# Performance work log

Measured on AMD Instinct MI355X. Metric: run time of the kernel, lower is better.

The kernel has to match this reference:

```python
import jax, jax.numpy as jnp
import numpy as np

B, T, NH, NB = 16, 400, 100, 65
SR, BLOCK = 16000, 160
REV_LEN = SR  # Reverb(sampling_rate, sampling_rate)


def _fft_convolve(signal, kernel):
    # torch: pad signal right by n, kernel left by its length, multiply spectra, keep 2nd half
    n = signal.shape[-1]
    s = jnp.pad(signal, [(0, 0)] * (signal.ndim - 1) + [(0, n)])
    k = jnp.pad(kernel, [(0, 0)] * (kernel.ndim - 1) + [(kernel.shape[-1], 0)])
    out = jnp.fft.irfft(jnp.fft.rfft(s) * jnp.fft.rfft(k), s.shape[-1])
    return out[..., out.shape[-1] // 2:]


def _amp_to_impulse_response(amp, target_size):
    # amp: [..., n_bands] real magnitudes treated as zero-phase rfft coefficients
    ir = jnp.fft.irfft(jax.lax.complex(amp, jnp.zeros_like(amp)))  # [..., 2*(NB-1)]
    fs = ir.shape[-1]
    ir = jnp.roll(ir, fs // 2, axis=-1)
    win = 0.5 - 0.5 * jnp.cos(2.0 * np.pi * jnp.arange(fs, dtype=ir.dtype) / fs)  # periodic hann
    ir = ir * win
    ir = jnp.pad(ir, [(0, 0)] * (ir.ndim - 1) + [(0, target_size - fs)])
    return jnp.roll(ir, -fs // 2, axis=-1)


def setup_inputs() -> dict:
    key = jax.random.key(0)
    ks = jax.random.split(key, 6)
    pitch = 40.0 + 400.0 * jax.random.uniform(ks[0], (B, T, 1), dtype=jnp.float32)
    total_amp = jax.random.uniform(ks[1], (B, T), dtype=jnp.float32)
    harmo_amps = jax.random.uniform(ks[2], (B, NH, T), dtype=jnp.float32) + 1e-3
    noise_filter = 0.1 * jax.random.uniform(ks[3], (B, T, NB), dtype=jnp.float32)
    noise = 2.0 * jax.random.uniform(ks[4], (B, T, BLOCK), dtype=jnp.float32) - 1.0
    reverb_noise = 2.0 * jax.random.uniform(ks[5], (REV_LEN, 1), dtype=jnp.float32) - 1.0
    decay = jnp.asarray(5.0, jnp.float32)
    wet = jnp.asarray(0.0, jnp.float32)
    return dict(pitch=pitch, total_amp=total_amp, harmo_amps=harmo_amps,
                noise_filter=noise_filter, noise=noise, reverb_noise=reverb_noise,
                decay=decay, wet=wet, sampling_rate=SR, block_size=BLOCK)


def reference(pitch, total_amp, harmo_amps, noise_filter, noise, reverb_noise,
              decay, wet, sampling_rate, block_size):
    dt = pitch.dtype
    n_harm = harmo_amps.shape[1]
    harm_idx = jnp.arange(1, n_harm + 1, dtype=dt)
    # remove_above_nyquist: mask harmonics whose freq >= sr/2 (tiny epsilon kept, as in DDSP)
    freqs = pitch[:, :, 0][:, None, :] * harm_idx[None, :, None]          # [B,NH,T]
    aa = (freqs < (sampling_rate / 2)).astype(dt) + 1e-4
    amps = harmo_amps * aa
    amps = jnp.transpose(amps, (0, 2, 1))                                  # [B,T,NH]
    amps = amps / jnp.sum(amps, axis=-1, keepdims=True)
    amps = amps * total_amp[..., None]
    # nearest-neighbor upsample by block_size (F.interpolate default mode)
    amps_up = jnp.repeat(amps, block_size, axis=1)                         # [B,N,NH]
    pitch_up = jnp.repeat(pitch, block_size, axis=1)                       # [B,N,1]
    # harmonic additive synthesis
    omega = jnp.cumsum(2.0 * np.pi * pitch_up / sampling_rate, axis=1)     # [B,N,1]
    harmonic = jnp.sum(jnp.sin(omega * harm_idx) * amps_up, axis=-1, keepdims=True)
    # filtered noise branch
    impulse = _amp_to_impulse_response(noise_filter, block_size)           # [B,T,BLOCK]
    noise_f = _fft_convolve(noise, impulse)                                # [B,T,BLOCK]
    noise_f = noise_f.reshape(noise_f.shape[0], -1, 1)                     # [B,N,1]
    signal = harmonic + noise_f
    # reverb (forward with reverb=True)
    rev_len = reverb_noise.shape[0]
    t = (jnp.arange(rev_len, dtype=dt) / sampling_rate)[None, :, None]     # [1,L,1]
    imp = reverb_noise[None] * jnp.exp(-jax.nn.softplus(-decay) * t * 500.0) * jax.nn.sigmoid(wet)
    imp = imp.at[:, 0].set(1.0)
    imp = jnp.pad(imp, ((0, 0), (0, signal.shape[1] - rev_len), (0, 0)))   # [1,N,1]
    out = _fft_convolve(signal[..., 0], imp[..., 0])[..., None]            # [B,N,1]
    return out
```

## Files before the change

### kernel.cpp

```cpp
#include <hip/hip_runtime.h>

#define B_ 16
#define T_ 400
#define NH_ 100
#define NB_ 65
#define BLK_ 160
#define SR_ 16000
#define N_ 64000
#define REV_ 16000
#define KPAD_ 16128
#define KTOT_ 80128
#define M_ 16
#define NWG_ 250
#define ISTRIDE_ 16768

typedef __attribute__((ext_vector_type(8))) _Float16 f16x8;
typedef __attribute__((ext_vector_type(2))) _Float16 f16x2;
typedef __attribute__((ext_vector_type(4))) float f32x4;
typedef __attribute__((ext_vector_type(4))) unsigned uint4v;
typedef uint4v __attribute__((aligned(4))) uint4v_a4;

static __device__ __forceinline__ float dot2f(f16x2 a, f16x2 b, float c) {
#if __has_builtin(__builtin_amdgcn_fdot2)
  return __builtin_amdgcn_fdot2(a, b, c, false);
#else
  return fmaf((float)a[0], (float)b[0], fmaf((float)a[1], (float)b[1], c));
#endif
}

__global__ __launch_bounds__(512) void k_pre(const float* __restrict__ pitch,
                                             const float* __restrict__ rn,
                                             const float* __restrict__ dec,
                                             const float* __restrict__ wet,
                                             double* __restrict__ Pv,
                                             double* __restrict__ Xv,
                                             _Float16* __restrict__ IMPREV,
                                             _Float16* __restrict__ PH) {
  const int blk = blockIdx.x, tid = threadIdx.x;
  if (blk < 66) {
    const int gid = blk * 512 + tid;
    if (gid < 2 * ISTRIDE_) {
      const int c = gid / ISTRIDE_, u = gid - c * ISTRIDE_;
      const int i = 16383 - u - c;
      float v = 0.f;
      if (i == 0) {
        v = 1.0f;
      } else if (i > 0 && i < REV_) {
        const float a = log1pf(expf(-dec[0]));
        const float sg = 1.f / (1.f + expf(-wet[0]));
        v = rn[i] * expf(-a * ((float)i / (float)SR_) * 500.0f) * sg;
      }
      IMPREV[gid] = (_Float16)v;
    }
    return;
  }
  if (blk < 129) {
    const int gid = (blk - 66) * 512 + tid;
    ((f32x4*)PH)[gid] = (f32x4){0.f, 0.f, 0.f, 0.f};
    return;
  }
  __shared__ double s[512];
  const int b = blk - 129, t = tid;
  double x = 0.0;
  if (t < T_) x = (double)pitch[b * T_ + t] * (1.0 / (double)SR_);
  s[t] = x;
  __syncthreads();
  for (int off = 1; off < 512; off <<= 1) {
    double v = (t >= off) ? s[t - off] : 0.0;
    __syncthreads();
    s[t] += v;
    __syncthreads();
  }
  if (t < T_) {
    Xv[b * T_ + t] = x;
    Pv[b * T_ + t] = (s[t] - x) * 160.0;
  }
}

__global__ __launch_bounds__(320) void k_synth(
    const float* __restrict__ pitch, const float* __restrict__ tamp,
    const float* __restrict__ harmo, const float* __restrict__ nfilt,
    const float* __restrict__ noise, const double* __restrict__ Pv,
    const double* __restrict__ Xv, _Float16* __restrict__ PH) {
  const int tid = threadIdx.x;
  const int g = (tid >= 160) ? 1 : 0;
  const int ltid = tid - (g << 7) - (g << 5);
  const int bt = (blockIdx.x << 1) + g;
  const int b = bt / T_, t = bt - b * T_;
  __shared__ __align__(16) float amp[2][112];
  __shared__ __align__(16) float a_s[2][68];
  __shared__ __align__(16) float ir_s[2][68];
  __shared__ __align__(16) _Float16 C0[2][320];
  __shared__ __align__(16) _Float16 C1[2][320];
  __shared__ __align__(16) _Float16 imp_sw[2][128];
  __shared__ float red_s[2];

  const float pv = pitch[bt];
  int nv = (int)(8000.0f / pv);
  if (nv > NH_) nv = NH_;
  while (nv < NH_ && (float)(nv + 1) * pv < 8000.0f) ++nv;
  while (nv > 0 && (float)nv * pv >= 8000.0f) --nv;

  if (ltid < NB_) a_s[g][ltid] = nfilt[bt * NB_ + ltid];
  {
    const _Float16 nh = (_Float16)noise[bt * BLK_ + ltid];
    C0[g][160 + ltid] = nh;
    C1[g][159 + ltid] = nh;
    C0[g][ltid] = (_Float16)0.f;
    if (ltid < 159) C1[g][ltid] = (_Float16)0.f;
  }
  if (ltid < NH_) {
    const float ha = harmo[(b * NH_ + ltid) * T_ + t];
    const float aa = (pv * (float)(ltid + 1) < 8000.0f ? 1.0f : 0.0f) + 1e-4f;
    amp[g][ltid] = ha * aa;
  } else if (ltid < 112) {
    amp[g][ltid] = 0.f;
  }
  __syncthreads();

  float irv = 0.f;
  if (ltid < 65) {
    const float phi = (float)ltid * (1.0f / 128.0f);
    const float c1 = __builtin_amdgcn_cosf(phi);
    const float c2 = fmaf(2.f * c1, c1, -1.f);
    const float c3 = fmaf(2.f * c2, c1, -c1);
    const float c4 = fmaf(2.f * c2, c2, -1.f);
    const float tc = 2.f * c4;
    float x0 = 1.f, p0 = c4;
    float x1 = c1, p1 = c3;
    float x2 = c2, p2 = c2;
    float x3 = c3, p3 = c1;
    float a0 = 0.f, a1 = 0.f, a2 = 0.f, a3 = 0.f;
#pragma unroll
    for (int m = 0; m < 8; ++m) {
      const f32x4 aA = *(const f32x4*)&a_s[g][m << 3];
      const f32x4 aB = *(const f32x4*)&a_s[g][(m << 3) + 4];
      a0 = fmaf(aA[0], x0, a0); const float y0 = fmaf(tc, x0, -p0);
      a1 = fmaf(aA[1], x1, a1); const float y1 = fmaf(tc, x1, -p1);
      a2 = fmaf(aA[2], x2, a2); const float y2 = fmaf(tc, x2, -p2);
      a3 = fmaf(aA[3], x3, a3); const float y3 = fmaf(tc, x3, -p3);
      a0 = fmaf(aB[0], y0, a0); const float z0 = fmaf(tc, y0, -x0); p0 = y0; x0 = z0;
      a1 = fmaf(aB[1], y1, a1); const float z1 = fmaf(tc, y1, -x1); p1 = y1; x1 = z1;
      a2 = fmaf(aB[2], y2, a2); const float z2 = fmaf(tc, y2, -x2); p2 = y2; x2 = z2;
      a3 = fmaf(aB[3], y3, a3); const float z3 = fmaf(tc, y3, -x3); p3 = y3; x3 = z3;
    }
    const float accS = (a0 + a1) + (a2 + a3);
    irv = (2.f * accS - a_s[g][0] + ((ltid & 1) ? -a_s[g][64] : a_s[g][64])) * (1.0f / 128.0f);
    ir_s[g][ltid] = irv;
  } else if (ltid >= 128) {
    const int l = ltid - 128;
    float v = amp[g][l] + amp[g][l + 32] + amp[g][l + 64] + (l < 4 ? amp[g][l + 96] : 0.f);
    v += __shfl_xor(v, 16);
    v += __shfl_xor(v, 8);
    v += __shfl_xor(v, 4);
    v += __shfl_xor(v, 2);
    v += __shfl_xor(v, 1);
    if (l == 0) red_s[g] = v;
  }
  __syncthreads();

  if (ltid < 64) {
    const float w = 0.5f + 0.5f * __builtin_amdgcn_cosf((float)ltid * (1.0f / 128.0f));
    imp_sw[g][ltid ^ 1] = (_Float16)(w * irv);
  } else if (ltid >= 96 && ltid < 160) {
    const int u = ltid - 96;
    const float w = 0.5f - 0.5f * __builtin_amdgcn_cosf((float)u * (1.0f / 128.0f));
    imp_sw[g][64 + (u ^ 1)] = (_Float16)(w * ir_s[g][64 - u]);
  }
  const float scale = tamp[bt] / red_s[g];
  double th = Pv[bt] + (double)(ltid + 1) * Xv[bt];
  th -= floor(th);
  const float theta = (float)th;
  const float cT = __builtin_amdgcn_cosf(theta);
  const float sT = __builtin_amdgcn_sinf(theta);
  __syncthreads();

  float acc;
  {
    const float c2 = fmaf(cT, cT, -sT * sT);
    const float s2 = 2.f * cT * sT;
    const float s3 = fmaf(s2, cT, c2 * sT);
    const float s4 = 2.f * s2 * c2;
    const float c4 = fmaf(2.f * c2, c2, -1.f);
    const float tc = 2.f * c4;
    float x0 = sT, p0 = -s3;
    float x1 = s2, p1 = -s2;
    float x2 = s3, p2 = -sT;
    float x3 = s4, p3 = 0.f;
    float a0 = 0.f, a1 = 0.f, a2 = 0.f, a3 = 0.f;
    const int S = (nv + 7) >> 3;
    for (int m = 0; m < S; ++m) {
      const f32x4 aA = *(const f32x4*)&amp[g][m << 3];
      const f32x4 aB = *(const f32x4*)&amp[g][(m << 3) + 4];
      a0 = fmaf(aA[0], x0, a0); const float y0 = fmaf(tc, x0, -p0);
      a1 = fmaf(aA[1], x1, a1); const float y1 = fmaf(tc, x1, -p1);
      a2 = fmaf(aA[2], x2, a2); const float y2 = fmaf(tc, x2, -p2);
      a3 = fmaf(aA[3], x3, a3); const float y3 = fmaf(tc, x3, -p3);
      a0 = fmaf(aB[0], y0, a0); const float z0 = fmaf(tc, y0, -x0); p0 = y0; x0 = z0;
      a1 = fmaf(aB[1], y1, a1); const float z1 = fmaf(tc, y1, -x1); p1 = y1; x1 = z1;
      a2 = fmaf(aB[2], y2, a2); const float z2 = fmaf(tc, y2, -x2); p2 = y2; x2 = z2;
      a3 = fmaf(aB[3], y3, a3); const float z3 = fmaf(tc, y3, -x3); p3 = y3; x3 = z3;
    }
    acc = ((a0 + a1) + (a2 + a3)) * scale;
  }

  float nf = 0.f;
  {
    const f16x2* np0;
    int pe;
    if (ltid & 1) {
      np0 = (const f16x2*)C0[g];
      pe = (159 + ltid) >> 1;
    } else {
      np0 = (const f16x2*)C1[g];
      pe = (158 + ltid) >> 1;
    }
    const f16x8* ip = (const f16x8*)imp_sw[g];
#pragma unroll
    for (int k0 = 0; k0 < 8; ++k0) {
      const f16x8 i8 = ip[k0];
      const int kb = k0 << 2;
      nf = dot2f((f16x2){i8[0], i8[1]}, np0[pe - kb], nf);
      nf = dot2f((f16x2){i8[2], i8[3]}, np0[pe - kb - 1], nf);
      nf = dot2f((f16x2){i8[4], i8[5]}, np0[pe - kb - 2], nf);
      nf = dot2f((f16x2){i8[6], i8[7]}, np0[pe - kb - 3], nf);
    }
#pragma unroll
    for (int k0 = 0; k0 < 8; ++k0) {
      const f16x8 i8 = ip[8 + k0];
      const int kb = (k0 << 2) + 48;
      nf = dot2f((f16x2){i8[0], i8[1]}, np0[pe - kb], nf);
      nf = dot2f((f16x2){i8[2], i8[3]}, np0[pe - kb - 1], nf);
      nf = dot2f((f16x2){i8[4], i8[5]}, np0[pe - kb - 2], nf);
      nf = dot2f((f16x2){i8[6], i8[7]}, np0[pe - kb - 3], nf);
    }
  }

  const float v = acc + nf;
  const unsigned k = (unsigned)(KPAD_ + t * BLK_ + ltid);
  const unsigned off = ((k >> 3) << 7) + ((unsigned)b << 3) + (k & 7u);
  PH[off] = (_Float16)v;
}

static __device__ __forceinline__ f32x4 mfma_f16(f16x8 a, f16x8 b, f32x4 c) {
  return __builtin_amdgcn_mfma_f32_16x16x32_f16(a, b, c, 0, 0, 0);
}

static __device__ __forceinline__ f16x8 lfrag(const unsigned short* __restrict__ base, int byteoff) {
  union { uint4v u; f16x8 v; } x;
  x.u = *(const uint4v_a4*)((const char*)base + byteoff);
  return x.v;
}

template <int U, bool ISSUE, bool CONSUME>
__device__ __forceinline__ void conv_step(f16x8 (&Rh)[M_], f32x4 (&acc)[M_], f16x8 (&bhi2)[2],
                                          f16x8 (&nb)[4], f16x8 (&na0)[4], f16x8 (&na1)[4],
                                          const f16x8* __restrict__ ph,
                                          const unsigned short* __restrict__ abase,
                                          int& kit, int& abyte) {
  if (ISSUE) {
    kit += 64;
    nb[U & 3] = ph[kit];
    abyte += 64;
    na0[U & 3] = lfrag(abase, abyte);
    na1[U & 3] = lfrag(abase, abyte - 32);
  }
#pragma unroll
  for (int mm = 0; mm < M_; ++mm) {
    const int m = (mm + M_ - 2) & (M_ - 1);
    const int sl = (m - 2 * U) & (M_ - 1);
    acc[m] = mfma_f16(Rh[sl], bhi2[U & 1], acc[m]);
  }
  if (CONSUME) {
    Rh[(M_ - 2 - 2 * U) & (M_ - 1)] = na0[(U + 1) & 3];
    Rh[(M_ - 1 - 2 * U) & (M_ - 1)] = na1[(U + 1) & 3];
    bhi2[(U + 1) & 1] = nb[(U + 1) & 3];
  }
}

__global__ __launch_bounds__(512) void k_mconv(const unsigned short* __restrict__ IMPREV,
                                               const f16x8* __restrict__ PH,
                                               float* __restrict__ out) {
  const int tid = threadIdx.x;
  const int s = tid >> 6, lane = tid & 63;
  int w = blockIdx.x;
  {
    const int q = NWG_ / 8, r = NWG_ % 8;
    const int xcd = w & 7, o = w >> 3;
    w = (xcd < r ? xcd * (q + 1) : r * (q + 1) + (xcd - r) * q) + o;
  }
  const int Q0 = w << 8;
  const int T0 = 1022 - 128 * s;

  const int pat = (lane & 15) - ((lane >> 4) << 3);
  const int o0 = 16223 - 16 * T0 - pat;
  const int par = o0 & 1;
  const unsigned short* abase = IMPREV + (par ? ISTRIDE_ : 0);
  int abyte = 2 * (384 + o0 - par);

  f16x8 Rh[M_];
#pragma unroll
  for (int m = 0; m < M_; ++m) Rh[m] = lfrag(abase, abyte - 32 * m);
  f32x4 acc[M_];
#pragma unroll
  for (int m = 0; m < M_; ++m) acc[m] = (f32x4){0.f, 0.f, 0.f, 0.f};

  const f16x8* ph = PH + ((lane >> 4) << 4) + (lane & 15);
  int kit = (Q0 + 2048 * s) << 1;
  f16x8 bhi2[2], nb[4], na0[4], na1[4];
  bhi2[0] = ph[kit];
  kit += 64; nb[1] = ph[kit]; abyte += 64; na0[1] = lfrag(abase, abyte); na1[1] = lfrag(abase, abyte - 32);
  kit += 64; nb[2] = ph[kit]; abyte += 64; na0[2] = lfrag(abase, abyte); na1[2] = lfrag(abase, abyte - 32);
  kit += 64; nb[3] = ph[kit]; abyte += 64; na0[3] = lfrag(abase, abyte); na1[3] = lfrag(abase, abyte - 32);

  for (int ii = 0; ii < 7; ++ii) {
    conv_step<0, true, true>(Rh, acc, bhi2, nb, na0, na1, ph, abase, kit, abyte);
    conv_step<1, true, true>(Rh, acc, bhi2, nb, na0, na1, ph, abase, kit, abyte);
    conv_step<2, true, true>(Rh, acc, bhi2, nb, na0, na1, ph, abase, kit, abyte);
    conv_step<3, true, true>(Rh, acc, bhi2, nb, na0, na1, ph, abase, kit, abyte);
    conv_step<4, true, true>(Rh, acc, bhi2, nb, na0, na1, ph, abase, kit, abyte);
    conv_step<5, true, true>(Rh, acc, bhi2, nb, na0, na1, ph, abase, kit, abyte);
    conv_step<6, true, true>(Rh, acc, bhi2, nb, na0, na1, ph, abase, kit, abyte);
    conv_step<7, true, true>(Rh, acc, bhi2, nb, na0, na1, ph, abase, kit, abyte);
  }
  conv_step<0, true, true>(Rh, acc, bhi2, nb, na0, na1, ph, abase, kit, abyte);
  conv_step<1, true, true>(Rh, acc, bhi2, nb, na0, na1, ph, abase, kit, abyte);
  conv_step<2, true, true>(Rh, acc, bhi2, nb, na0, na1, ph, abase, kit, abyte);
  conv_step<3, true, true>(Rh, acc, bhi2, nb, na0, na1, ph, abase, kit, abyte);
  conv_step<4, false, true>(Rh, acc, bhi2, nb, na0, na1, ph, abase, kit, abyte);
  conv_step<5, false, true>(Rh, acc, bhi2, nb, na0, na1, ph, abase, kit, abyte);
  conv_step<6, false, true>(Rh, acc, bhi2, nb, na0, na1, ph, abase, kit, abyte);
  conv_step<7, false, false>(Rh, acc, bhi2, nb, na0, na1, ph, abase, kit, abyte);

  __shared__ f32x4 part[4][M_][64];
  if (s < 4) {
#pragma unroll
    for (int m = 0; m < M_; ++m) part[s][m][lane] = acc[m];
  }
  __syncthreads();
  if (s >= 4) {
#pragma unroll
    for (int m = 0; m < M_; ++m) part[s - 4][m][lane] += acc[m];
  }
  __syncthreads();
#pragma unroll
  for (int half = 0; half < 2; ++half) {
    const int it = tid + (half << 9);
    const int m = it >> 6, ln = it & 63;
    f32x4 v = part[0][m][ln];
    v += part[1][m][ln];
    v += part[2][m][ln];
    v += part[3][m][ln];
    const int b = ln & 15, gq = ln >> 4;
    *(f32x4*)(out + (size_t)b * N_ + Q0 + (m << 4) + (gq << 2)) = v;
  }
}

extern "C" void kernel_launch(void* const* d_in, const int* in_sizes, int n_in,
                              void* d_out, int out_size, void* d_ws, size_t ws_size,
                              hipStream_t stream) {
  const float* pitch = (const float*)d_in[0];
  const float* tamp  = (const float*)d_in[1];
  const float* harmo = (const float*)d_in[2];
  const float* nfilt = (const float*)d_in[3];
  const float* noise = (const float*)d_in[4];
  const float* rn    = (const float*)d_in[5];
  const float* dec   = (const float*)d_in[6];
  const float* wet   = (const float*)d_in[7];

  char* ws = (char*)d_ws;
  size_t off = 0;
  _Float16* PH = (_Float16*)(ws + off);     off += (size_t)KTOT_ * 16 * 2;
  _Float16* IMPREV = (_Float16*)(ws + off); off += (size_t)2 * ISTRIDE_ * 2;
  double* Pv = (double*)(ws + off);         off += (size_t)B_ * T_ * 8;
  double* Xv = (double*)(ws + off);         off += (size_t)B_ * T_ * 8;
  float* out = (float*)d_out;

  k_pre<<<dim3(145), dim3(512), 0, stream>>>(pitch, rn, dec, wet, Pv, Xv, IMPREV, PH);
  k_synth<<<dim3(B_ * T_ / 2), dim3(320), 0, stream>>>(pitch, tamp, harmo, nfilt, noise, Pv, Xv, PH);
  k_mconv<<<dim3(NWG_), dim3(512), 0, stream>>>((const unsigned short*)IMPREV, (const f16x8*)PH, out);
}
```

Before: 58.08 us.

## Switch reverb Toeplitz convolution to 32x32x16 MFMA tiles

```diff
diff --git a/kernel.cpp b/kernel.cpp
--- a/kernel.cpp
+++ b/kernel.cpp
@@ -10,13 +10,14 @@
 #define REV_ 16000
 #define KPAD_ 16128
 #define KTOT_ 80128
-#define M_ 16
+#define KTOT2_ 80160
 #define NWG_ 250
 #define ISTRIDE_ 16768
 
 typedef __attribute__((ext_vector_type(8))) _Float16 f16x8;
 typedef __attribute__((ext_vector_type(2))) _Float16 f16x2;
 typedef __attribute__((ext_vector_type(4))) float f32x4;
+typedef __attribute__((ext_vector_type(16))) float f32x16;
 typedef __attribute__((ext_vector_type(4))) unsigned uint4v;
 typedef uint4v __attribute__((aligned(4))) uint4v_a4;
 
@@ -54,13 +55,17 @@
     }
     return;
   }
-  if (blk < 129) {
+  if (blk < 130) {
     const int gid = (blk - 66) * 512 + tid;
-    ((f32x4*)PH)[gid] = (f32x4){0.f, 0.f, 0.f, 0.f};
+    if (gid < 32256) {
+      ((f32x4*)PH)[gid] = (f32x4){0.f, 0.f, 0.f, 0.f};
+    } else if (gid < 32320) {
+      ((f32x4*)PH)[160256 + gid - 32256] = (f32x4){0.f, 0.f, 0.f, 0.f};
+    }
     return;
   }
   __shared__ double s[512];
-  const int b = blk - 129, t = tid;
+  const int b = blk - 130, t = tid;
   double x = 0.0;
   if (t < T_) x = (double)pitch[b * T_ + t] * (1.0 / (double)SR_);
   s[t] = x;
@@ -242,8 +247,8 @@
   PH[off] = (_Float16)v;
 }
 
-static __device__ __forceinline__ f32x4 mfma_f16(f16x8 a, f16x8 b, f32x4 c) {
-  return __builtin_amdgcn_mfma_f32_16x16x32_f16(a, b, c, 0, 0, 0);
+static __device__ __forceinline__ f32x16 mfma32(f16x8 a, f16x8 b, f32x16 c) {
+  return __builtin_amdgcn_mfma_f32_32x32x16_f16(a, b, c, 0, 0, 0);
 }
 
 static __device__ __forceinline__ f16x8 lfrag(const unsigned short* __restrict__ base, int byteoff) {
@@ -253,28 +258,24 @@
 }
 
 template <int U, bool ISSUE, bool CONSUME>
-__device__ __forceinline__ void conv_step(f16x8 (&Rh)[M_], f32x4 (&acc)[M_], f16x8 (&bhi2)[2],
-                                          f16x8 (&nb)[4], f16x8 (&na0)[4], f16x8 (&na1)[4],
-                                          const f16x8* __restrict__ ph,
-                                          const unsigned short* __restrict__ abase,
-                                          int& kit, int& abyte) {
+__device__ __forceinline__ void cstep(f16x8 (&Rng)[16], f32x16 (&acc)[4], f16x8& bhi,
+                                      f16x8 (&na)[4], f16x8 (&nbB)[4],
+                                      const f16x8* __restrict__ phB,
+                                      const unsigned short* __restrict__ abase,
+                                      int& kitB, int& abyteA) {
   if (ISSUE) {
-    kit += 64;
-    nb[U & 3] = ph[kit];
-    abyte += 64;
-    na0[U & 3] = lfrag(abase, abyte);
-    na1[U & 3] = lfrag(abase, abyte - 32);
-  }
-#pragma unroll
-  for (int mm = 0; mm < M_; ++mm) {
-    const int m = (mm + M_ - 2) & (M_ - 1);
-    const int sl = (m - 2 * U) & (M_ - 1);
-    acc[m] = mfma_f16(Rh[sl], bhi2[U & 1], acc[m]);
-  }
+    abyteA += 32;
+    na[U & 3] = lfrag(abase, abyteA);
+    kitB += 32;
+    nbB[U & 3] = phB[kitB];
+  }
+  acc[0] = mfma32(Rng[U & 15], bhi, acc[0]);
+  acc[1] = mfma32(Rng[(U + 12) & 15], bhi, acc[1]);
+  acc[2] = mfma32(Rng[(U + 8) & 15], bhi, acc[2]);
+  acc[3] = mfma32(Rng[(U + 4) & 15], bhi, acc[3]);
   if (CONSUME) {
-    Rh[(M_ - 2 - 2 * U) & (M_ - 1)] = na0[(U + 1) & 3];
-    Rh[(M_ - 1 - 2 * U) & (M_ - 1)] = na1[(U + 1) & 3];
-    bhi2[(U + 1) & 1] = nb[(U + 1) & 3];
+    Rng[(U + 1) & 15] = na[(U + 1) & 3];
+    bhi = nbB[(U + 1) & 3];
   }
 }
 
@@ -290,69 +291,98 @@
     w = (xcd < r ? xcd * (q + 1) : r * (q + 1) + (xcd - r) * q) + o;
   }
   const int Q0 = w << 8;
-  const int T0 = 1022 - 128 * s;
-
-  const int pat = (lane & 15) - ((lane >> 4) << 3);
-  const int o0 = 16223 - 16 * T0 - pat;
-  const int par = o0 & 1;
-  const unsigned short* abase = IMPREV + (par ? ISTRIDE_ : 0);
-  int abyte = 2 * (384 + o0 - par);
-
-  f16x8 Rh[M_];
-#pragma unroll
-  for (int m = 0; m < M_; ++m) Rh[m] = lfrag(abase, abyte - 32 * m);
-  f32x4 acc[M_];
-#pragma unroll
-  for (int m = 0; m < M_; ++m) acc[m] = (f32x4){0.f, 0.f, 0.f, 0.f};
-
-  const f16x8* ph = PH + ((lane >> 4) << 4) + (lane & 15);
-  int kit = (Q0 + 2048 * s) << 1;
-  f16x8 bhi2[2], nb[4], na0[4], na1[4];
-  bhi2[0] = ph[kit];
-  kit += 64; nb[1] = ph[kit]; abyte += 64; na0[1] = lfrag(abase, abyte); na1[1] = lfrag(abase, abyte - 32);
-  kit += 64; nb[2] = ph[kit]; abyte += 64; na0[2] = lfrag(abase, abyte); na1[2] = lfrag(abase, abyte - 32);
-  kit += 64; nb[3] = ph[kit]; abyte += 64; na0[3] = lfrag(abase, abyte); na1[3] = lfrag(abase, abyte - 32);
+
+  const int c = (lane & 1) ^ 1;
+  const unsigned short* abase = IMPREV + (c ? ISTRIDE_ : 0);
+  const int u0 = 255 + 2048 * s - (lane & 31) + 8 * (lane >> 5) - c;
+  const int A0 = 2 * u0;
+
+  f16x8 Rng[16];
+  Rng[0] = lfrag(abase, A0);
+#pragma unroll
+  for (int k = 1; k < 4; ++k) Rng[k] = (f16x8)((_Float16)0.f);
+#pragma unroll
+  for (int k = 4; k < 16; ++k) Rng[k] = lfrag(abase, A0 + 32 * k - 512);
+
+  f32x16 acc[4];
+#pragma unroll
+  for (int q = 0; q < 4; ++q) acc[q] = (f32x16)(0.f);
+
+  const f16x8* phB = PH + 16 * (lane >> 5) + 64 * ((lane >> 4) & 1) + (lane & 15);
+  const int kB0 = (Q0 + 2048 * s) << 1;
+  f16x8 bhi = phB[kB0];
+  f16x8 na[4], nbB[4];
+  na[1] = lfrag(abase, A0 + 32);  nbB[1] = phB[kB0 + 32];
+  na[2] = lfrag(abase, A0 + 64);  nbB[2] = phB[kB0 + 64];
+  na[3] = lfrag(abase, A0 + 96);  nbB[3] = phB[kB0 + 96];
+  int abyteA = A0 + 96;
+  int kitB = kB0 + 96;
 
   for (int ii = 0; ii < 7; ++ii) {
-    conv_step<0, true, true>(Rh, acc, bhi2, nb, na0, na1, ph, abase, kit, abyte);
-    conv_step<1, true, true>(Rh, acc, bhi2, nb, na0, na1, ph, abase, kit, abyte);
-    conv_step<2, true, true>(Rh, acc, bhi2, nb, na0, na1, ph, abase, kit, abyte);
-    conv_step<3, true, true>(Rh, acc, bhi2, nb, na0, na1, ph, abase, kit, abyte);
-    conv_step<4, true, true>(Rh, acc, bhi2, nb, na0, na1, ph, abase, kit, abyte);
-    conv_step<5, true, true>(Rh, acc, bhi2, nb, na0, na1, ph, abase, kit, abyte);
-    conv_step<6, true, true>(Rh, acc, bhi2, nb, na0, na1, ph, abase, kit, abyte);
-    conv_step<7, true, true>(Rh, acc, bhi2, nb, na0, na1, ph, abase, kit, abyte);
-  }
-  conv_step<0, true, true>(Rh, acc, bhi2, nb, na0, na1, ph, abase, kit, abyte);
-  conv_step<1, true, true>(Rh, acc, bhi2, nb, na0, na1, ph, abase, kit, abyte);
-  conv_step<2, true, true>(Rh, acc, bhi2, nb, na0, na1, ph, abase, kit, abyte);
-  conv_step<3, true, true>(Rh, acc, bhi2, nb, na0, na1, ph, abase, kit, abyte);
-  conv_step<4, false, true>(Rh, acc, bhi2, nb, na0, na1, ph, abase, kit, abyte);
-  conv_step<5, false, true>(Rh, acc, bhi2, nb, na0, na1, ph, abase, kit, abyte);
-  conv_step<6, false, true>(Rh, acc, bhi2, nb, na0, na1, ph, abase, kit, abyte);
-  conv_step<7, false, false>(Rh, acc, bhi2, nb, na0, na1, ph, abase, kit, abyte);
-
-  __shared__ f32x4 part[4][M_][64];
+    cstep<0, true, true>(Rng, acc, bhi, na, nbB, phB, abase, kitB, abyteA);
+    cstep<1, true, true>(Rng, acc, bhi, na, nbB, phB, abase, kitB, abyteA);
+    cstep<2, true, true>(Rng, acc, bhi, na, nbB, phB, abase, kitB, abyteA);
+    cstep<3, true, true>(Rng, acc, bhi, na, nbB, phB, abase, kitB, abyteA);
+    cstep<4, true, true>(Rng, acc, bhi, na, nbB, phB, abase, kitB, abyteA);
+    cstep<5, true, true>(Rng, acc, bhi, na, nbB, phB, abase, kitB, abyteA);
+    cstep<6, true, true>(Rng, acc, bhi, na, nbB, phB, abase, kitB, abyteA);
+    cstep<7, true, true>(Rng, acc, bhi, na, nbB, phB, abase, kitB, abyteA);
+    cstep<8, true, true>(Rng, acc, bhi, na, nbB, phB, abase, kitB, abyteA);
+    cstep<9, true, true>(Rng, acc, bhi, na, nbB, phB, abase, kitB, abyteA);
+    cstep<10, true, true>(Rng, acc, bhi, na, nbB, phB, abase, kitB, abyteA);
+    cstep<11, true, true>(Rng, acc, bhi, na, nbB, phB, abase, kitB, abyteA);
+    cstep<12, true, true>(Rng, acc, bhi, na, nbB, phB, abase, kitB, abyteA);
+    cstep<13, true, true>(Rng, acc, bhi, na, nbB, phB, abase, kitB, abyteA);
+    cstep<14, true, true>(Rng, acc, bhi, na, nbB, phB, abase, kitB, abyteA);
+    cstep<15, true, true>(Rng, acc, bhi, na, nbB, phB, abase, kitB, abyteA);
+  }
+  cstep<0, true, true>(Rng, acc, bhi, na, nbB, phB, abase, kitB, abyteA);
+  cstep<1, true, true>(Rng, acc, bhi, na, nbB, phB, abase, kitB, abyteA);
+  cstep<2, true, true>(Rng, acc, bhi, na, nbB, phB, abase, kitB, abyteA);
+  cstep<3, true, true>(Rng, acc, bhi, na, nbB, phB, abase, kitB, abyteA);
+  cstep<4, true, true>(Rng, acc, bhi, na, nbB, phB, abase, kitB, abyteA);
+  cstep<5, true, true>(Rng, acc, bhi, na, nbB, phB, abase, kitB, abyteA);
+  cstep<6, true, true>(Rng, acc, bhi, na, nbB, phB, abase, kitB, abyteA);
+  cstep<7, true, true>(Rng, acc, bhi, na, nbB, phB, abase, kitB, abyteA);
+  cstep<8, true, true>(Rng, acc, bhi, na, nbB, phB, abase, kitB, abyteA);
+  cstep<9, true, true>(Rng, acc, bhi, na, nbB, phB, abase, kitB, abyteA);
+  cstep<10, true, true>(Rng, acc, bhi, na, nbB, phB, abase, kitB, abyteA);
+  cstep<11, true, true>(Rng, acc, bhi, na, nbB, phB, abase, kitB, abyteA);
+  cstep<12, false, true>(Rng, acc, bhi, na, nbB, phB, abase, kitB, abyteA);
+  cstep<13, false, true>(Rng, acc, bhi, na, nbB, phB, abase, kitB, abyteA);
+  cstep<14, false, true>(Rng, acc, bhi, na, nbB, phB, abase, kitB, abyteA);
+  cstep<15, false, false>(Rng, acc, bhi, na, nbB, phB, abase, kitB, abyteA);
+
+  __shared__ f32x4 part[4][4][4][64];
   if (s < 4) {
 #pragma unroll
-    for (int m = 0; m < M_; ++m) part[s][m][lane] = acc[m];
+    for (int q = 0; q < 4; ++q)
+#pragma unroll
+      for (int rg = 0; rg < 4; ++rg)
+        part[s][q][rg][lane] =
+            (f32x4){acc[q][4 * rg], acc[q][4 * rg + 1], acc[q][4 * rg + 2], acc[q][4 * rg + 3]};
   }
   __syncthreads();
   if (s >= 4) {
 #pragma unroll
-    for (int m = 0; m < M_; ++m) part[s - 4][m][lane] += acc[m];
+    for (int q = 0; q < 4; ++q)
+#pragma unroll
+      for (int rg = 0; rg < 4; ++rg)
+        part[s - 4][q][rg][lane] +=
+            (f32x4){acc[q][4 * rg], acc[q][4 * rg + 1], acc[q][4 * rg + 2], acc[q][4 * rg + 3]};
   }
   __syncthreads();
 #pragma unroll
   for (int half = 0; half < 2; ++half) {
     const int it = tid + (half << 9);
-    const int m = it >> 6, ln = it & 63;
-    f32x4 v = part[0][m][ln];
-    v += part[1][m][ln];
-    v += part[2][m][ln];
-    v += part[3][m][ln];
-    const int b = ln & 15, gq = ln >> 4;
-    *(f32x4*)(out + (size_t)b * N_ + Q0 + (m << 4) + (gq << 2)) = v;
+    const int ln = it & 63, rg = (it >> 6) & 3, q = it >> 8;
+    f32x4 v = part[0][q][rg][ln];
+    v += part[1][q][rg][ln];
+    v += part[2][q][rg][ln];
+    v += part[3][q][rg][ln];
+    const int b = ln & 15;
+    const int pos = Q0 + 64 * q + 32 * ((ln >> 4) & 1) + 8 * rg + 4 * (ln >> 5);
+    *(f32x4*)(out + (size_t)b * N_ + pos) = v;
   }
 }
 
@@ -370,13 +400,13 @@
 
   char* ws = (char*)d_ws;
   size_t off = 0;
-  _Float16* PH = (_Float16*)(ws + off);     off += (size_t)KTOT_ * 16 * 2;
+  _Float16* PH = (_Float16*)(ws + off);     off += (size_t)KTOT2_ * 16 * 2;
   _Float16* IMPREV = (_Float16*)(ws + off); off += (size_t)2 * ISTRIDE_ * 2;
   double* Pv = (double*)(ws + off);         off += (size_t)B_ * T_ * 8;
   double* Xv = (double*)(ws + off);         off += (size_t)B_ * T_ * 8;
   float* out = (float*)d_out;
 
-  k_pre<<<dim3(145), dim3(512), 0, stream>>>(pitch, rn, dec, wet, Pv, Xv, IMPREV, PH);
+  k_pre<<<dim3(146), dim3(512), 0, stream>>>(pitch, rn, dec, wet, Pv, Xv, IMPREV, PH);
   k_synth<<<dim3(B_ * T_ / 2), dim3(320), 0, stream>>>(pitch, tamp, harmo, nfilt, noise, Pv, Xv, PH);
   k_mconv<<<dim3(NWG_), dim3(512), 0, stream>>>((const unsigned short*)IMPREV, (const f16x8*)PH, out);
 }
```

Result: slower. 63.75 us (+9.8%).
